# Optimization experiments

Hardware: AMD Instinct MI355X
Metric: run time of the kernel (lower is better)

## Reference

```python
import jax, jax.numpy as jnp
import numpy as np

K = 3
PAD = 1


def _conv_offset(x, w_off, b_off):
    # standard 3x3 conv, stride 1, pad 1, with bias -> [B, 18, H, W]
    y = jax.lax.conv_general_dilated(
        x, w_off, window_strides=(1, 1), padding=((PAD, PAD), (PAD, PAD)),
        dimension_numbers=('NCHW', 'OIHW', 'NCHW'))
    return y + b_off[None, :, None, None]


def _deform_conv(x, offset, w_dcn):
    # x: [B,Cin,H,W], offset: [B,2*K*K,H,W] (dy,dx interleaved per tap), w_dcn: [Cout,Cin,K,K]
    B, Cin, H, W = x.shape
    KK = K * K
    Ho, Wo = offset.shape[2], offset.shape[3]

    ky = jnp.repeat(jnp.arange(K), K)          # [KK] kernel row index
    kx = jnp.tile(jnp.arange(K), K)            # [KK] kernel col index
    off = offset.reshape(B, KK, 2, Ho, Wo)
    dy, dx = off[:, :, 0], off[:, :, 1]        # [B,KK,Ho,Wo]

    gy = (jnp.arange(Ho)[None, :, None] - PAD + ky[:, None, None]).astype(x.dtype)  # [KK,Ho,1]
    gx = (jnp.arange(Wo)[None, None, :] - PAD + kx[:, None, None]).astype(x.dtype)  # [KK,1,Wo]
    py = gy[None] + dy                         # [B,KK,Ho,Wo] sampling rows
    px = gx[None] + dx                         # [B,KK,Ho,Wo] sampling cols

    y0 = jnp.floor(py); x0 = jnp.floor(px)
    wy1 = py - y0; wx1 = px - x0
    wy0 = 1.0 - wy1; wx0 = 1.0 - wx1

    x_flat = x.reshape(B, Cin, H * W)

    def gather(yi, xi, wgt):
        valid = (yi >= 0) & (yi <= H - 1) & (xi >= 0) & (xi <= W - 1)
        yc = jnp.clip(yi, 0, H - 1).astype(jnp.int32)
        xc = jnp.clip(xi, 0, W - 1).astype(jnp.int32)
        idx = yc * W + xc                      # [B,KK,Ho,Wo]
        vals = jax.vmap(lambda xb, ib: xb[:, ib])(x_flat, idx)  # [B,Cin,KK,Ho,Wo]
        w = (wgt * valid.astype(x.dtype))[:, None]              # [B,1,KK,Ho,Wo]
        return vals * w

    sampled = (gather(y0, x0, wy0 * wx0)
               + gather(y0, x0 + 1, wy0 * wx1)
               + gather(y0 + 1, x0, wy1 * wx0)
               + gather(y0 + 1, x0 + 1, wy1 * wx1))  # [B,Cin,KK,Ho,Wo]

    wr = w_dcn.reshape(w_dcn.shape[0], Cin, KK)
    return jnp.einsum('bckhw,ock->bohw', sampled, wr)


def setup_inputs() -> dict:
    key = jax.random.key(0)
    k1, k2, k3, k4 = jax.random.split(key, 4)
    B, Cin, H, W = 8, 32, 160, 160
    Cout = 32
    x = jax.random.normal(k1, (B, Cin, H, W), jnp.float32)
    w_off = jax.random.normal(k2, (2 * K * K, Cin, K, K), jnp.float32) * 0.01
    b_off = jax.random.normal(k3, (2 * K * K,), jnp.float32) * 0.01
    w_dcn = jax.random.normal(k4, (Cout, Cin, K, K), jnp.float32) * 0.1
    return {'x': x, 'w_off': w_off, 'b_off': b_off, 'w_dcn': w_dcn}


def reference(x, w_off, b_off, w_dcn):
    offset = _conv_offset(x, w_off, b_off)
    y = _deform_conv(x, offset, w_dcn)
    return jax.nn.relu(y)
```

## Files before the change

kernel.cpp:

```cpp
#include <hip/hip_runtime.h>

#define H_ 160
#define W_ 160
#define HW_ (H_ * W_)
#define NPIX (8 * HW_)


typedef __attribute__((ext_vector_type(8)))  short  short8;
typedef __attribute__((ext_vector_type(4)))  float  f32x4;
typedef __attribute__((ext_vector_type(2)))  float  f32x2;
typedef __attribute__((ext_vector_type(16))) float  f32x16;
typedef __attribute__((ext_vector_type(4)))  unsigned u32x4;

__device__ __forceinline__ unsigned short bf16_rne(float f) {
    unsigned u = __float_as_uint(f);
    u += 0x7fffu + ((u >> 16) & 1u);
    return (unsigned short)(u >> 16);
}
__device__ __forceinline__ unsigned pack2_bf16(float a, float b) {
    unsigned ua = __float_as_uint(a); ua += 0x7fffu + ((ua >> 16) & 1u);
    unsigned ub = __float_as_uint(b); ub += 0x7fffu + ((ub >> 16) & 1u);
    return (ua >> 16) | (ub & 0xffff0000u);
}
__device__ __forceinline__ f32x2 up2(unsigned u) {
    f32x2 r;
    r.x = __uint_as_float(u << 16);
    r.y = __uint_as_float(u & 0xffff0000u);
    return r;
}

__global__ __launch_bounds__(256) void nhwc_bf16(
    const float* __restrict__ x, unsigned short* __restrict__ xT)
{
    const int pix = blockIdx.x * 256 + threadIdx.x;
    const int p = pix % HW_;
    const int b = pix / HW_;
    const float* __restrict__ src = x + (size_t)b * 32 * HW_ + p;
    unsigned* __restrict__ dst = (unsigned*)(xT + (size_t)pix * 32);
    #pragma unroll
    for (int g = 0; g < 16; ++g)
        dst[g] = pack2_bf16(src[(2 * g) * HW_], src[(2 * g + 1) * HW_]);
}

__global__ __launch_bounds__(256, 4) void dcn_offset_mfma(
    const unsigned short* __restrict__ xT,
    const float* __restrict__ w_off,
    const float* __restrict__ b_off,
    float* __restrict__ off_ws)
{
    __shared__ __align__(16) unsigned short wl[9 * 2 * 64 * 8];
    __shared__ float bl[32];
    const int tid = threadIdx.x;
    for (int d = tid; d < 9 * 1024; d += 256) {
        const int tap = d >> 10, r = d & 1023, j = r >> 5, c = r & 31;
        const int s = c >> 4, kg = (c >> 3) & 1;
        const int unit = (tap * 2 + s) * 64 + j + 32 * kg;
        wl[unit * 8 + (c & 7)] =
            (j < 18) ? bf16_rne(w_off[(j * 32 + c) * 9 + tap]) : (unsigned short)0;
    }
    if (tid < 32) bl[tid] = (tid < 18) ? b_off[tid] : 0.0f;
    __syncthreads();

    const int wave = tid >> 6, lane = tid & 63;
    const int n = lane & 31;
    const int hh = lane >> 5;
    const int pixbase = blockIdx.x * 128 + wave * 32;
    const int pix = pixbase + n;
    const int w = pix % W_, h = (pix / W_) % H_, b = pix / HW_;
    const unsigned short* __restrict__ xb = xT + (size_t)b * HW_ * 32 + hh * 8;

    f32x16 acc = {};
    const u32x4 z4 = {0u, 0u, 0u, 0u};

    #pragma unroll
    for (int tap = 0; tap < 9; ++tap) {
        const int yy = h - 1 + tap / 3;
        const int xx = w - 1 + tap % 3;
        const bool valid = (yy >= 0) && (yy < H_) && (xx >= 0) && (xx < W_);
        const int idx = min(max(yy, 0), H_ - 1) * W_ + min(max(xx, 0), W_ - 1);
        const unsigned short* __restrict__ p = xb + (size_t)idx * 32;
        u32x4 l0 = *(const u32x4*)(p);
        u32x4 l1 = *(const u32x4*)(p + 16);
        l0 = valid ? l0 : z4;
        l1 = valid ? l1 : z4;
        const short8 a0 = __builtin_bit_cast(short8, l0);
        const short8 a1 = __builtin_bit_cast(short8, l1);
        const short8 b0 = *(const short8*)(wl + ((tap * 2 + 0) * 64 + lane) * 8);
        const short8 b1 = *(const short8*)(wl + ((tap * 2 + 1) * 64 + lane) * 8);
        acc = __builtin_amdgcn_mfma_f32_32x32x16_bf16(a0, b0, acc, 0, 0, 0);
        acc = __builtin_amdgcn_mfma_f32_32x32x16_bf16(a1, b1, acc, 0, 0, 0);
    }

    if (n < 18) {
        const float bia = bl[n];
        float* __restrict__ op = off_ws + (size_t)n * NPIX + pixbase + 4 * hh;
        #pragma unroll
        for (int g = 0; g < 4; ++g) {
            f32x4 r;
            #pragma unroll
            for (int i = 0; i < 4; ++i) r[i] = acc[g * 4 + i] + bia;
            *(f32x4*)(op + g * 8) = r;
        }
    }
}

__global__ __launch_bounds__(256, 4) void dcn_sample_mfma(
    const unsigned short* __restrict__ xT,
    const float* __restrict__ w_dcn,
    const float* __restrict__ off_ws,
    float* __restrict__ out)
{
    __shared__ __align__(16) unsigned short wl[9 * 2 * 64 * 8];
    const int tid = threadIdx.x;
    for (int d = tid; d < 9 * 1024; d += 256) {
        const int tap = d >> 10, r = d & 1023, o = r >> 5, c = r & 31;
        const int s = c >> 4, kg = (c >> 3) & 1;
        const int unit = (tap * 2 + s) * 64 + o + 32 * kg;
        wl[unit * 8 + (c & 7)] = bf16_rne(w_dcn[(o * 32 + c) * 9 + tap]);
    }
    __syncthreads();

    const int wave = tid >> 6, lane = tid & 63;
    const int n = lane & 31;
    const int hh = lane >> 5;
    const int pixbase = blockIdx.x * 128 + wave * 32;
    const int pix = pixbase + n;
    const int w = pix % W_, h = (pix / W_) % H_, b = pix / HW_;
    const unsigned short* __restrict__ xb = xT + (size_t)b * HW_ * 32 + hh * 8;

    f32x16 acc = {};

    #pragma unroll
    for (int tap = 0; tap < 9; ++tap) {
        const float dy = off_ws[(2 * tap) * NPIX + pix];
        const float dx = off_ws[(2 * tap + 1) * NPIX + pix];
        const float py = (float)(h - 1 + tap / 3) + dy;
        const float px = (float)(w - 1 + tap % 3) + dx;
        const float fy0 = floorf(py), fx0 = floorf(px);
        const float wy1 = py - fy0, wx1 = px - fx0;
        const float wy0 = 1.0f - wy1, wx0 = 1.0f - wx1;
        const int y0 = (int)fy0, x0 = (int)fx0;
        const bool vy0 = (y0 >= 0) && (y0 < H_);
        const bool vy1 = (y0 + 1 >= 0) && (y0 + 1 < H_);
        const bool vx0 = (x0 >= 0) && (x0 < W_);
        const bool vx1 = (x0 + 1 >= 0) && (x0 + 1 < W_);
        const float w00 = (vy0 && vx0) ? wy0 * wx0 : 0.0f;
        const float w01 = (vy0 && vx1) ? wy0 * wx1 : 0.0f;
        const float w10 = (vy1 && vx0) ? wy1 * wx0 : 0.0f;
        const float w11 = (vy1 && vx1) ? wy1 * wx1 : 0.0f;
        const int yc0 = min(max(y0, 0), H_ - 1), yc1 = min(max(y0 + 1, 0), H_ - 1);
        const int xc0 = min(max(x0, 0), W_ - 1), xc1 = min(max(x0 + 1, 0), W_ - 1);

        const unsigned short* __restrict__ pA = xb + (size_t)(yc0 * W_ + xc0) * 32;
        const unsigned short* __restrict__ pB = xb + (size_t)(yc0 * W_ + xc1) * 32;
        const unsigned short* __restrict__ pC = xb + (size_t)(yc1 * W_ + xc0) * 32;
        const unsigned short* __restrict__ pD = xb + (size_t)(yc1 * W_ + xc1) * 32;
        const u32x4 A0 = *(const u32x4*)(pA);      const u32x4 A1 = *(const u32x4*)(pA + 16);
        const u32x4 B0 = *(const u32x4*)(pB);      const u32x4 B1 = *(const u32x4*)(pB + 16);
        const u32x4 C0 = *(const u32x4*)(pC);      const u32x4 C1 = *(const u32x4*)(pC + 16);
        const u32x4 D0 = *(const u32x4*)(pD);      const u32x4 D1 = *(const u32x4*)(pD + 16);

        #define COMB(a, bb, cc, dd) ({ \
            const f32x2 v = up2(a) * w00 + up2(bb) * w01 + up2(cc) * w10 + up2(dd) * w11; \
            pack2_bf16(v.x, v.y); })
        u32x4 av0, av1;
        av0.x = COMB(A0.x, B0.x, C0.x, D0.x);
        av0.y = COMB(A0.y, B0.y, C0.y, D0.y);
        av0.z = COMB(A0.z, B0.z, C0.z, D0.z);
        av0.w = COMB(A0.w, B0.w, C0.w, D0.w);
        av1.x = COMB(A1.x, B1.x, C1.x, D1.x);
        av1.y = COMB(A1.y, B1.y, C1.y, D1.y);
        av1.z = COMB(A1.z, B1.z, C1.z, D1.z);
        av1.w = COMB(A1.w, B1.w, C1.w, D1.w);
        #undef COMB

        const short8 a0 = __builtin_bit_cast(short8, av0);
        const short8 a1 = __builtin_bit_cast(short8, av1);
        const short8 b0 = *(const short8*)(wl + ((tap * 2 + 0) * 64 + lane) * 8);
        const short8 b1 = *(const short8*)(wl + ((tap * 2 + 1) * 64 + lane) * 8);
        acc = __builtin_amdgcn_mfma_f32_32x32x16_bf16(a0, b0, acc, 0, 0, 0);
        acc = __builtin_amdgcn_mfma_f32_32x32x16_bf16(a1, b1, acc, 0, 0, 0);
    }

    float* __restrict__ ob = out + (size_t)b * 32 * HW_ + (size_t)n * HW_
                           + (pixbase - b * HW_) + 4 * hh;
    #pragma unroll
    for (int g = 0; g < 4; ++g) {
        f32x4 r;
        #pragma unroll
        for (int i = 0; i < 4; ++i) r[i] = fmaxf(acc[g * 4 + i], 0.0f);
        *(f32x4*)(ob + g * 8) = r;
    }
}

extern "C" void kernel_launch(void* const* d_in, const int* in_sizes, int n_in,
                              void* d_out, int out_size, void* d_ws, size_t ws_size,
                              hipStream_t stream) {
    const float* x     = (const float*)d_in[0];
    const float* w_off = (const float*)d_in[1];
    const float* b_off = (const float*)d_in[2];
    const float* w_dcn = (const float*)d_in[3];
    float* out = (float*)d_out;

    unsigned short* xT = (unsigned short*)d_ws;
    float* off_ws = (float*)((char*)d_ws + (size_t)NPIX * 32 * 2);

    nhwc_bf16<<<800, 256, 0, stream>>>(x, xT);
    dcn_offset_mfma<<<1600, 256, 0, stream>>>(xT, w_off, b_off, off_ws);
    dcn_sample_mfma<<<1600, 256, 0, stream>>>(xT, w_dcn, off_ws, out);
}
```

Before: 159.7 us.

## Fuse offset conv and deformable sampling into one kernel via LDS offsets

Merges the offset-convolution kernel and the deformable sampling kernel into a single kernel. Each wave computes its 18 offset channels for 32 pixels, writes them to a padded LDS tile, and reads them back for bilinear sampling. This removes the global offset workspace round-trip (about 18 floats per pixel written then read) and one kernel launch. The cost is more LDS per block for two weight tables plus the offset tile, a lower occupancy hint (3 instead of 4), and both weight tables being reloaded per block.

```diff
diff --git a/kernel.cpp b/kernel.cpp
--- a/kernel.cpp
+++ b/kernel.cpp
@@ -42,21 +42,25 @@
         dst[g] = pack2_bf16(src[(2 * g) * HW_], src[(2 * g + 1) * HW_]);
 }
 
-__global__ __launch_bounds__(256, 4) void dcn_offset_mfma(
+__global__ __launch_bounds__(256, 3) void dcn_fused(
     const unsigned short* __restrict__ xT,
     const float* __restrict__ w_off,
     const float* __restrict__ b_off,
-    float* __restrict__ off_ws)
+    const float* __restrict__ w_dcn,
+    float* __restrict__ out)
 {
-    __shared__ __align__(16) unsigned short wl[9 * 2 * 64 * 8];
+    __shared__ __align__(16) unsigned short wo[9 * 2 * 64 * 8];
+    __shared__ __align__(16) unsigned short wd[9 * 2 * 64 * 8];
+    __shared__ float offl[4 * 18 * 33];
     __shared__ float bl[32];
     const int tid = threadIdx.x;
     for (int d = tid; d < 9 * 1024; d += 256) {
         const int tap = d >> 10, r = d & 1023, j = r >> 5, c = r & 31;
         const int s = c >> 4, kg = (c >> 3) & 1;
         const int unit = (tap * 2 + s) * 64 + j + 32 * kg;
-        wl[unit * 8 + (c & 7)] =
-            (j < 18) ? bf16_rne(w_off[(j * 32 + c) * 9 + tap]) : (unsigned short)0;
+        wo[unit * 8 + (c & 7)] = (j < 18) ? bf16_rne(w_off[(j * 32 + c) * 9 + tap])
+                                          : (unsigned short)0;
+        wd[unit * 8 + (c & 7)] = bf16_rne(w_dcn[(j * 32 + c) * 9 + tap]);
     }
     if (tid < 32) bl[tid] = (tid < 18) ? b_off[tid] : 0.0f;
     __syncthreads();
@@ -69,71 +73,46 @@
     const int w = pix % W_, h = (pix / W_) % H_, b = pix / HW_;
     const unsigned short* __restrict__ xb = xT + (size_t)b * HW_ * 32 + hh * 8;
 
-    f32x16 acc = {};
-    const u32x4 z4 = {0u, 0u, 0u, 0u};
-
-    #pragma unroll
-    for (int tap = 0; tap < 9; ++tap) {
-        const int yy = h - 1 + tap / 3;
-        const int xx = w - 1 + tap % 3;
-        const bool valid = (yy >= 0) && (yy < H_) && (xx >= 0) && (xx < W_);
-        const int idx = min(max(yy, 0), H_ - 1) * W_ + min(max(xx, 0), W_ - 1);
-        const unsigned short* __restrict__ p = xb + (size_t)idx * 32;
-        u32x4 l0 = *(const u32x4*)(p);
-        u32x4 l1 = *(const u32x4*)(p + 16);
-        l0 = valid ? l0 : z4;
-        l1 = valid ? l1 : z4;
-        const short8 a0 = __builtin_bit_cast(short8, l0);
-        const short8 a1 = __builtin_bit_cast(short8, l1);
-        const short8 b0 = *(const short8*)(wl + ((tap * 2 + 0) * 64 + lane) * 8);
-        const short8 b1 = *(const short8*)(wl + ((tap * 2 + 1) * 64 + lane) * 8);
-        acc = __builtin_amdgcn_mfma_f32_32x32x16_bf16(a0, b0, acc, 0, 0, 0);
-        acc = __builtin_amdgcn_mfma_f32_32x32x16_bf16(a1, b1, acc, 0, 0, 0);
-    }
-
-    if (n < 18) {
-        const float bia = bl[n];
-        float* __restrict__ op = off_ws + (size_t)n * NPIX + pixbase + 4 * hh;
+    {
+        f32x16 acc = {};
+        const u32x4 z4 = {0u, 0u, 0u, 0u};
         #pragma unroll
-        for (int g = 0; g < 4; ++g) {
-            f32x4 r;
+        for (int tap = 0; tap < 9; ++tap) {
+            const int yy = h - 1 + tap / 3;
+            const int xx = w - 1 + tap % 3;
+            const bool valid = (yy >= 0) && (yy < H_) && (xx >= 0) && (xx < W_);
+            const int idx = min(max(yy, 0), H_ - 1) * W_ + min(max(xx, 0), W_ - 1);
+            const unsigned short* __restrict__ px_ = xb + (size_t)idx * 32;
+            u32x4 l0 = *(const u32x4*)(px_);
+            u32x4 l1 = *(const u32x4*)(px_ + 16);
+            l0 = valid ? l0 : z4;
+            l1 = valid ? l1 : z4;
+            const short8 a0 = __builtin_bit_cast(short8, l0);
+            const short8 a1 = __builtin_bit_cast(short8, l1);
+            const short8 b0 = *(const short8*)(wo + ((tap * 2 + 0) * 64 + lane) * 8);
+            const short8 b1 = *(const short8*)(wo + ((tap * 2 + 1) * 64 + lane) * 8);
+            acc = __builtin_amdgcn_mfma_f32_32x32x16_bf16(a0, b0, acc, 0, 0, 0);
+            acc = __builtin_amdgcn_mfma_f32_32x32x16_bf16(a1, b1, acc, 0, 0, 0);
+        }
+        float* __restrict__ owp = offl + wave * 594;
+        if (n < 18) {
+            const float bia = bl[n];
             #pragma unroll
-            for (int i = 0; i < 4; ++i) r[i] = acc[g * 4 + i] + bia;
-            *(f32x4*)(op + g * 8) = r;
+            for (int r = 0; r < 16; ++r) {
+                const int prow = (r & 3) + 8 * (r >> 2) + 4 * hh;
+                owp[n * 33 + prow] = acc[r] + bia;
+            }
         }
-    }
-}
-
-__global__ __launch_bounds__(256, 4) void dcn_sample_mfma(
-    const unsigned short* __restrict__ xT,
-    const float* __restrict__ w_dcn,
-    const float* __restrict__ off_ws,
-    float* __restrict__ out)
-{
-    __shared__ __align__(16) unsigned short wl[9 * 2 * 64 * 8];
-    const int tid = threadIdx.x;
-    for (int d = tid; d < 9 * 1024; d += 256) {
-        const int tap = d >> 10, r = d & 1023, o = r >> 5, c = r & 31;
-        const int s = c >> 4, kg = (c >> 3) & 1;
-        const int unit = (tap * 2 + s) * 64 + o + 32 * kg;
-        wl[unit * 8 + (c & 7)] = bf16_rne(w_dcn[(o * 32 + c) * 9 + tap]);
     }
     __syncthreads();
 
-    const int wave = tid >> 6, lane = tid & 63;
-    const int n = lane & 31;
-    const int hh = lane >> 5;
-    const int pixbase = blockIdx.x * 128 + wave * 32;
-    const int pix = pixbase + n;
-    const int w = pix % W_, h = (pix / W_) % H_, b = pix / HW_;
-    const unsigned short* __restrict__ xb = xT + (size_t)b * HW_ * 32 + hh * 8;
-
+    const float* __restrict__ ow = offl + wave * 594;
     f32x16 acc = {};
 
     #pragma unroll
     for (int tap = 0; tap < 9; ++tap) {
-        const float dy = off_ws[(2 * tap) * NPIX + pix];
-        const float dx = off_ws[(2 * tap + 1) * NPIX + pix];
+        const float dy = ow[(2 * tap) * 33 + n];
+        const float dx = ow[(2 * tap + 1) * 33 + n];
         const float py = (float)(h - 1 + tap / 3) + dy;
         const float px = (float)(w - 1 + tap % 3) + dx;
         const float fy0 = floorf(py), fx0 = floorf(px);
@@ -176,8 +155,8 @@
 
         const short8 a0 = __builtin_bit_cast(short8, av0);
         const short8 a1 = __builtin_bit_cast(short8, av1);
-        const short8 b0 = *(const short8*)(wl + ((tap * 2 + 0) * 64 + lane) * 8);
-        const short8 b1 = *(const short8*)(wl + ((tap * 2 + 1) * 64 + lane) * 8);
+        const short8 b0 = *(const short8*)(wd + ((tap * 2 + 0) * 64 + lane) * 8);
+        const short8 b1 = *(const short8*)(wd + ((tap * 2 + 1) * 64 + lane) * 8);
         acc = __builtin_amdgcn_mfma_f32_32x32x16_bf16(a0, b0, acc, 0, 0, 0);
         acc = __builtin_amdgcn_mfma_f32_32x32x16_bf16(a1, b1, acc, 0, 0, 0);
     }
@@ -203,9 +182,7 @@
     float* out = (float*)d_out;
 
     unsigned short* xT = (unsigned short*)d_ws;
-    float* off_ws = (float*)((char*)d_ws + (size_t)NPIX * 32 * 2);
 
     nhwc_bf16<<<800, 256, 0, stream>>>(x, xT);
-    dcn_offset_mfma<<<1600, 256, 0, stream>>>(xT, w_off, b_off, off_ws);
-    dcn_sample_mfma<<<1600, 256, 0, stream>>>(xT, w_dcn, off_ws, out);
+    dcn_fused<<<1600, 256, 0, stream>>>(xT, w_off, b_off, w_dcn, out);
 }
```

New measurement: 157.9 us. About the same (-1.1%).
